# Optimization experiments

Hardware: AMD Instinct MI355X
Metric: run time of the kernel (lower is better)

Reference implementation:

```python
import jax, jax.numpy as jnp
import numpy as np

DIM = 512
NUM_HEADS = 8
HEAD_DIM = DIM // NUM_HEADS
B, S = 2, 2048


def setup_inputs() -> dict:
    key = jax.random.key(0)
    ks = jax.random.split(key, 16)
    scale = 1.0 / np.sqrt(DIM)
    inp = {
        "x": jax.random.normal(ks[0], (B, S, DIM), dtype=jnp.float32),
        "Qexpl": jax.random.normal(ks[1], (B, S, DIM), dtype=jnp.float32),
        "Kexpl": jax.random.normal(ks[2], (B, S, DIM), dtype=jnp.float32),
        "fl": jax.random.uniform(ks[3], (B,), dtype=jnp.float32),
        "fu": jax.random.uniform(ks[4], (B,), dtype=jnp.float32),
        "age": jax.random.uniform(ks[5], (B,), dtype=jnp.float32),
        "gender": jax.random.uniform(ks[6], (B,), dtype=jnp.float32),
        # Linear params: weight stored as [out, in] like torch; y = x @ W.T + b
        "Wq": jax.random.normal(ks[7], (DIM, DIM), dtype=jnp.float32) * scale,
        "bq": jnp.zeros((DIM,), dtype=jnp.float32),
        "Wk": jax.random.normal(ks[8], (DIM, DIM), dtype=jnp.float32) * scale,
        "bk": jnp.zeros((DIM,), dtype=jnp.float32),
        "Wv": jax.random.normal(ks[9], (DIM, DIM), dtype=jnp.float32) * scale,
        "bv": jnp.zeros((DIM,), dtype=jnp.float32),
        "Wo": jax.random.normal(ks[10], (DIM, DIM), dtype=jnp.float32) * scale,
        "bo": jnp.zeros((DIM,), dtype=jnp.float32),
    }
    return inp


def reference(x, Qexpl, Kexpl, fl, fu, age, gender, Wq, bq, Wk, bk, Wv, bv, Wo, bo):
    # drofe_fn is None -> Q/K projections used directly.
    Q = Qexpl @ Wq.T + bq            # [B, S, D]
    K = Kexpl @ Wk.T + bk            # [B, S, D]
    V = x @ Wv.T + bv                # [B, S, D]

    def split_heads(t):  # [B, S, D] -> [B, H, S, hd]
        return t.reshape(B, S, NUM_HEADS, HEAD_DIM).transpose(0, 2, 1, 3)

    Qh, Kh, Vh = split_heads(Q), split_heads(K), split_heads(V)
    scale = 1.0 / np.sqrt(HEAD_DIM).astype(np.float32)
    scores = jnp.einsum("bhqd,bhkd->bhqk", Qh, Kh) * scale  # [B, H, S, S]
    weights = jax.nn.softmax(scores, axis=-1)
    attn = jnp.einsum("bhqk,bhkd->bhqd", weights, Vh)        # [B, H, S, hd]
    attn = attn.transpose(0, 2, 1, 3).reshape(B, S, DIM)
    return attn @ Wo.T + bo
```

## Files before the change

kernel.cpp:

```cpp
#include <hip/hip_runtime.h>
#include <hip/hip_bf16.h>

typedef unsigned short ushort_t;
typedef __attribute__((ext_vector_type(8))) short bf16x8;
typedef __attribute__((ext_vector_type(4))) float f32x4;

__device__ __forceinline__ ushort_t f2bf(float f) {
    union { float f; unsigned u; } v; v.f = f;
    unsigned r = v.u + 0x7FFF + ((v.u >> 16) & 1);
    return (ushort_t)(r >> 16);
}
__device__ __forceinline__ float bfl(ushort_t u) {
    union { unsigned u; float f; } v; v.u = (unsigned)u << 16; return v.f;
}
__device__ __forceinline__ bf16x8 ld8(const ushort_t* p) { return *(const bf16x8*)p; }

__device__ __forceinline__ unsigned cvt2(float x, float y) {
    __hip_bfloat162 h = __float22bfloat162_rn(make_float2(x, y));
    unsigned r; __builtin_memcpy(&r, &h, 4); return r;
}
__device__ __forceinline__ bf16x8 pack8f(float4 a, float4 b) {
    union { unsigned u[4]; bf16x8 v; } o;
    o.u[0] = cvt2(a.x, a.y); o.u[1] = cvt2(a.z, a.w);
    o.u[2] = cvt2(b.x, b.y); o.u[3] = cvt2(b.z, b.w);
    return o.v;
}

__device__ __forceinline__ void gload_lds16(const ushort_t* g, ushort_t* l) {
    __builtin_amdgcn_global_load_lds(
        (const __attribute__((address_space(1))) void*)g,
        (__attribute__((address_space(3))) void*)l, 16, 0, 0);
}

__global__ __launch_bounds__(256, 2)
void proj_qkv_kernel(const float* __restrict__ Qe, const float* __restrict__ Ke,
                     const float* __restrict__ x,
                     const float* __restrict__ Wq, const float* __restrict__ Wk,
                     const float* __restrict__ Wv,
                     const float* __restrict__ bq, const float* __restrict__ bk,
                     const float* __restrict__ bv,
                     ushort_t* __restrict__ Qo, ushort_t* __restrict__ Ko,
                     ushort_t* __restrict__ Vt,
                     const float* __restrict__ Wo, ushort_t* __restrict__ Wob)
{
    const int z = blockIdx.z;
    if (z == 3) {
        int idx = ((blockIdx.y * 4 + blockIdx.x) * 256 + threadIdx.x) * 8;
        const float* s = Wo + idx;
        *(bf16x8*)(Wob + idx) = pack8f(*(const float4*)s, *(const float4*)(s + 4));
        return;
    }

    __shared__ ushort_t smem[2 * 128 * 72];
    ushort_t* lA = smem;
    ushort_t* lB = smem + 128 * 72;

    const float* A = (z == 0) ? Qe : (z == 1) ? Ke : x;
    const float* W = (z == 0) ? Wq : (z == 1) ? Wk : Wv;
    const float* bias = (z == 0) ? bq : (z == 1) ? bk : bv;

    const int m0 = blockIdx.y * 128, n0 = blockIdx.x * 128;
    const int t = threadIdx.x;
    const int lane = t & 63, wave = t >> 6;
    const int wm = (wave & 1) * 64, wn = (wave >> 1) * 64;
    const int fr = lane & 15, quad = lane >> 4;

    f32x4 acc[4][4] = {};
    float4 fa[4][2], fw[4][2];

#pragma unroll
    for (int i = 0; i < 4; ++i) {
        int s = i * 256 + t;
        int r = s >> 3, jp = s & 7;
        const float* pa = A + (size_t)(m0 + r) * 512 + jp * 8;
        fa[i][0] = *(const float4*)pa; fa[i][1] = *(const float4*)(pa + 4);
        const float* pw = W + (size_t)(n0 + r) * 512 + jp * 8;
        fw[i][0] = *(const float4*)pw; fw[i][1] = *(const float4*)(pw + 4);
    }

    for (int kk = 0; kk < 8; ++kk) {
        if (kk) __syncthreads();
#pragma unroll
        for (int i = 0; i < 4; ++i) {
            int s = i * 256 + t;
            int r = s >> 3, jp = s & 7;
            *(bf16x8*)(lA + r * 72 + jp * 8) = pack8f(fa[i][0], fa[i][1]);
            *(bf16x8*)(lB + r * 72 + jp * 8) = pack8f(fw[i][0], fw[i][1]);
        }
        __syncthreads();
        if (kk < 7) {
            int k0 = (kk + 1) * 64;
#pragma unroll
            for (int i = 0; i < 4; ++i) {
                int s = i * 256 + t;
                int r = s >> 3, jp = s & 7;
                const float* pa = A + (size_t)(m0 + r) * 512 + k0 + jp * 8;
                fa[i][0] = *(const float4*)pa; fa[i][1] = *(const float4*)(pa + 4);
                const float* pw = W + (size_t)(n0 + r) * 512 + k0 + jp * 8;
                fw[i][0] = *(const float4*)pw; fw[i][1] = *(const float4*)(pw + 4);
            }
        }

#pragma unroll
        for (int ks = 0; ks < 2; ++ks) {
            bf16x8 af[4], bfrag[4];
#pragma unroll
            for (int mt = 0; mt < 4; ++mt)
                af[mt] = ld8(lA + (wm + mt * 16 + fr) * 72 + (ks * 4 + quad) * 8);
#pragma unroll
            for (int nt = 0; nt < 4; ++nt)
                bfrag[nt] = ld8(lB + (wn + nt * 16 + fr) * 72 + (ks * 4 + quad) * 8);
#pragma unroll
            for (int mt = 0; mt < 4; ++mt)
#pragma unroll
                for (int nt = 0; nt < 4; ++nt)
                    acc[mt][nt] = __builtin_amdgcn_mfma_f32_16x16x32_bf16(
                        af[mt], bfrag[nt], acc[mt][nt], 0, 0, 0);
        }
    }

    const float C1 = 0.125f * 1.44269504088896340736f;
    if (z != 2) {
        ushort_t* dst = (z == 0) ? Qo : Ko;
#pragma unroll
        for (int nt = 0; nt < 4; ++nt) {
            int n = n0 + wn + nt * 16 + fr;
            float bb = bias[n];
#pragma unroll
            for (int mt = 0; mt < 4; ++mt) {
                int mb = m0 + wm + mt * 16 + quad * 4;
                if (z == 0) {
#pragma unroll
                    for (int r = 0; r < 4; ++r)
                        dst[(size_t)(mb + r) * 512 + n] = f2bf((acc[mt][nt][r] + bb) * C1);
                } else {
#pragma unroll
                    for (int r = 0; r < 4; ++r)
                        dst[(size_t)(mb + r) * 512 + n] = f2bf(acc[mt][nt][r] + bb);
                }
            }
        }
    } else {
        __syncthreads();
        ushort_t* lT = smem;
#pragma unroll
        for (int nt = 0; nt < 4; ++nt) {
            int nl = wn + nt * 16 + fr;
            float bb = bias[n0 + nl];
#pragma unroll
            for (int mt = 0; mt < 4; ++mt) {
                int tm = wm + mt * 16 + quad * 4;
#pragma unroll
                for (int r = 0; r < 4; ++r) {
                    int tl = tm + r;
                    int sg = (tl & 96) + ((tl & 12) << 1) + ((tl >> 4 & 1) << 2) + (tl & 3);
                    lT[nl * 136 + sg] = f2bf(acc[mt][nt][r] + bb);
                }
            }
        }
        __syncthreads();
        const int bidx = m0 >> 11, m0t = m0 & 2047;
#pragma unroll
        for (int i = 0; i < 8; ++i) {
            int s = i * 256 + t;
            int row = s >> 4, c = s & 15;
            int n = n0 + row;
            int h = n >> 6, d = n & 63;
            bf16x8 v = ld8(lT + row * 136 + c * 8);
            *(bf16x8*)(Vt + ((size_t)((bidx * 8 + h) * 64 + d)) * 2048 + m0t + c * 8) = v;
        }
    }
}

__global__ __launch_bounds__(256, 2)
void gemm_o_kernel(const ushort_t* __restrict__ Oh, const float* __restrict__ Lsum,
                   const ushort_t* __restrict__ W, const float* __restrict__ bias,
                   float* __restrict__ dst)
{
    __shared__ ushort_t lA[64 * 72];
    __shared__ ushort_t lB[64 * 72];
    const int m0 = blockIdx.y * 64, n0 = blockIdx.x * 64;
    const int t = threadIdx.x;
    const int lane = t & 63, wave = t >> 6;
    const int wm = (wave & 1) * 32, wn = (wave >> 1) * 32;
    const int fr = lane & 15, quad = lane >> 4;
    const int bq_ = m0 >> 11, qq0 = m0 & 2047;

    f32x4 acc[2][2] = {};
    bf16x8 va0[2], va1[2], vw[2];
    float l0[2], l1[2];

#pragma unroll
    for (int i = 0; i < 2; ++i) {
        int s = i * 256 + t;
        int r = s >> 3, jp = s & 7;
        va0[i] = ld8(Oh + (size_t)(m0 + r) * 512 + jp * 8);
        va1[i] = ld8(Oh + (size_t)(m0 + r + 4096) * 512 + jp * 8);
        l0[i] = Lsum[(bq_ * 8 + 0) * 2048 + qq0 + r];
        l1[i] = Lsum[((2 + bq_) * 8 + 0) * 2048 + qq0 + r];
        vw[i] = ld8(W + (size_t)(n0 + r) * 512 + jp * 8);
    }

    for (int kk = 0; kk < 8; ++kk) {
        if (kk) __syncthreads();
#pragma unroll
        for (int i = 0; i < 2; ++i) {
            int s = i * 256 + t;
            int r = s >> 3, jp = s & 7;
            float inv = 1.f / (l0[i] + l1[i]);
            union { bf16x8 v; ushort_t s8[8]; } a0, a1;
            a0.v = va0[i]; a1.v = va1[i];
            union { unsigned u[4]; bf16x8 v; } o;
#pragma unroll
            for (int j = 0; j < 4; ++j)
                o.u[j] = cvt2((bfl(a0.s8[2 * j]) + bfl(a1.s8[2 * j])) * inv,
                              (bfl(a0.s8[2 * j + 1]) + bfl(a1.s8[2 * j + 1])) * inv);
            *(bf16x8*)(lA + r * 72 + jp * 8) = o.v;
            *(bf16x8*)(lB + r * 72 + jp * 8) = vw[i];
        }
        __syncthreads();
        if (kk < 7) {
            int k0 = (kk + 1) * 64;
#pragma unroll
            for (int i = 0; i < 2; ++i) {
                int s = i * 256 + t;
                int r = s >> 3, jp = s & 7;
                va0[i] = ld8(Oh + (size_t)(m0 + r) * 512 + k0 + jp * 8);
                va1[i] = ld8(Oh + (size_t)(m0 + r + 4096) * 512 + k0 + jp * 8);
                l0[i] = Lsum[(bq_ * 8 + kk + 1) * 2048 + qq0 + r];
                l1[i] = Lsum[((2 + bq_) * 8 + kk + 1) * 2048 + qq0 + r];
                vw[i] = ld8(W + (size_t)(n0 + r) * 512 + k0 + jp * 8);
            }
        }

        bf16x8 af[2][2], bfrag[2][2];
#pragma unroll
        for (int ks = 0; ks < 2; ++ks) {
#pragma unroll
            for (int mt = 0; mt < 2; ++mt)
                af[mt][ks] = ld8(lA + (wm + mt * 16 + fr) * 72 + (ks * 4 + quad) * 8);
#pragma unroll
            for (int nt = 0; nt < 2; ++nt)
                bfrag[nt][ks] = ld8(lB + (wn + nt * 16 + fr) * 72 + (ks * 4 + quad) * 8);
        }
#pragma unroll
        for (int ks = 0; ks < 2; ++ks)
#pragma unroll
            for (int mt = 0; mt < 2; ++mt)
#pragma unroll
                for (int nt = 0; nt < 2; ++nt)
                    acc[mt][nt] = __builtin_amdgcn_mfma_f32_16x16x32_bf16(
                        af[mt][ks], bfrag[nt][ks], acc[mt][nt], 0, 0, 0);
    }

#pragma unroll
    for (int nt = 0; nt < 2; ++nt) {
        int n = n0 + wn + nt * 16 + fr;
        float bb = bias[n];
#pragma unroll
        for (int mt = 0; mt < 2; ++mt) {
            int mb = m0 + wm + mt * 16 + quad * 4;
#pragma unroll
            for (int r = 0; r < 4; ++r)
                dst[(size_t)(mb + r) * 512 + n] = acc[mt][nt][r] + bb;
        }
    }
}

__global__ __launch_bounds__(256, 4)
void attn_kernel(const ushort_t* __restrict__ Q, const ushort_t* __restrict__ K,
                 const ushort_t* __restrict__ Vt, ushort_t* __restrict__ Opart,
                 float* __restrict__ Lsum)
{
    __shared__ ushort_t lK[128 * 64];
    __shared__ ushort_t lV[64 * 128];

    const int b = blockIdx.z >> 1, half = blockIdx.z & 1;
    const int h = blockIdx.y;
    const int q0 = blockIdx.x * 64;
    const int kvbase = half * 1024;
    const int t = threadIdx.x;
    const int lane = t & 63, w = t >> 6;
    const int wq = w * 16;
    const int fr = lane & 15, quad = lane >> 4;
    const int fr7 = fr & 7;

    bf16x8 aq[2];
    {
        const ushort_t* qp = Q + (size_t)(b * 2048 + q0 + wq + fr) * 512 + h * 64 + quad * 8;
        aq[0] = ld8(qp);
        aq[1] = ld8(qp + 32);
    }

    const int krl = w * 32 + (lane >> 3);
    const ushort_t* kg = K + (size_t)(b * 2048 + kvbase + krl) * 512 + h * 64
                           + (lane & 7) * 8;
    ushort_t* lk_wr = lK + krl * 64 + (((lane & 7) ^ (krl & 7)) << 3);

    const int vrl = w * 4 + (lane >> 4);
    const ushort_t* vbase = Vt + (size_t)((b * 8 + h) * 64 + vrl) * 2048 + kvbase
                              + (((lane & 15) ^ (vrl & 7)) << 3);

    const ushort_t* kr0 = lK + fr * 64 + ((quad ^ fr7) << 3);
    const ushort_t* kr1 = lK + fr * 64 + (((4 + quad) ^ fr7) << 3);
    const ushort_t* vr0 = lV + fr * 128 + (((0 * 4 + quad) ^ fr7) << 3);
    const ushort_t* vr1 = lV + fr * 128 + (((1 * 4 + quad) ^ fr7) << 3);
    const ushort_t* vr2 = lV + fr * 128 + (((2 * 4 + quad) ^ fr7) << 3);
    const ushort_t* vr3 = lV + fr * 128 + (((3 * 4 + quad) ^ fr7) << 3);
    const ushort_t* vr[4] = { vr0, vr1, vr2, vr3 };

    bf16x8 kreg[4];
#pragma unroll
    for (int i = 0; i < 4; ++i)
        kreg[i] = ld8(kg + (size_t)(i * 8) * 512);
#pragma unroll
    for (int i = 0; i < 4; ++i)
        *(bf16x8*)(lk_wr + i * 8 * 64) = kreg[i];
    __syncthreads();

    f32x4 oacc[4] = {};
    float lsum = 0.f;

    for (int tt = 0; tt < 8; ++tt) {
        const int kv = tt << 7;

#pragma unroll
        for (int i = 0; i < 4; ++i)
            gload_lds16(vbase + kv + (size_t)(i * 16) * 2048, lV + (i * 16 + w * 4) * 128);
        __builtin_amdgcn_sched_barrier(0);
        if (tt < 7) {
#pragma unroll
            for (int i = 0; i < 4; ++i)
                kreg[i] = ld8(kg + (size_t)(kv + 128 + i * 8) * 512);
        }
        __builtin_amdgcn_sched_barrier(0);

        f32x4 sc[8] = {};
        __builtin_amdgcn_s_setprio(1);
#pragma unroll
        for (int nt = 0; nt < 8; ++nt) {
            bf16x8 kb = ld8(kr0 + nt * 16 * 64);
            sc[nt] = __builtin_amdgcn_mfma_f32_16x16x32_bf16(kb, aq[0], sc[nt], 0, 0, 0);
        }
#pragma unroll
        for (int nt = 0; nt < 8; ++nt) {
            bf16x8 kb = ld8(kr1 + nt * 16 * 64);
            sc[nt] = __builtin_amdgcn_mfma_f32_16x16x32_bf16(kb, aq[1], sc[nt], 0, 0, 0);
        }
        __builtin_amdgcn_s_setprio(0);

        if (tt < 7) asm volatile("s_waitcnt vmcnt(4)" ::: "memory");
        else        asm volatile("s_waitcnt vmcnt(0)" ::: "memory");
        __builtin_amdgcn_s_barrier();
        __builtin_amdgcn_sched_barrier(0);

        __builtin_amdgcn_s_setprio(1);
#pragma unroll
        for (int ks = 0; ks < 4; ++ks) {
            float p0[4], p1[4];
#pragma unroll
            for (int r = 0; r < 4; ++r) p0[r] = exp2f(sc[2 * ks][r]);
#pragma unroll
            for (int r = 0; r < 4; ++r) p1[r] = exp2f(sc[2 * ks + 1][r]);
            lsum += ((p0[0] + p0[1]) + (p0[2] + p0[3]))
                  + ((p1[0] + p1[1]) + (p1[2] + p1[3]));
            union { unsigned u[4]; bf16x8 v; } pa;
            pa.u[0] = cvt2(p0[0], p0[1]); pa.u[1] = cvt2(p0[2], p0[3]);
            pa.u[2] = cvt2(p1[0], p1[1]); pa.u[3] = cvt2(p1[2], p1[3]);
#pragma unroll
            for (int nt = 0; nt < 4; ++nt) {
                bf16x8 vb = ld8(vr[ks] + nt * 16 * 128);
                oacc[nt] = __builtin_amdgcn_mfma_f32_16x16x32_bf16(pa.v, vb, oacc[nt], 0, 0, 0);
            }
            if (ks == 0 && tt < 7) {
#pragma unroll
                for (int i = 0; i < 4; ++i)
                    *(bf16x8*)(lk_wr + i * 8 * 64) = kreg[i];
            }
        }
        __builtin_amdgcn_s_setprio(0);
        __syncthreads();
    }

    float rs = lsum;
    rs += __shfl_xor(rs, 16, 64);
    rs += __shfl_xor(rs, 32, 64);
#pragma unroll
    for (int r = 0; r < 4; ++r) {
        int qrow = q0 + wq + quad * 4 + r;
        ushort_t* od = Opart + ((size_t)(half * 2 + b) * 2048 + qrow) * 512 + h * 64;
#pragma unroll
        for (int nt = 0; nt < 4; ++nt)
            od[nt * 16 + fr] = f2bf(oacc[nt][r]);
    }
    if (lane < 16)
        Lsum[((half * 2 + b) * 8 + h) * 2048 + q0 + wq + lane] = rs;
}

extern "C" void kernel_launch(void* const* d_in, const int* in_sizes, int n_in,
                              void* d_out, int out_size, void* d_ws, size_t ws_size,
                              hipStream_t stream) {
    const float* x   = (const float*)d_in[0];
    const float* Qe  = (const float*)d_in[1];
    const float* Ke  = (const float*)d_in[2];
    const float* Wq  = (const float*)d_in[7];
    const float* bq  = (const float*)d_in[8];
    const float* Wk  = (const float*)d_in[9];
    const float* bk  = (const float*)d_in[10];
    const float* Wv  = (const float*)d_in[11];
    const float* bv  = (const float*)d_in[12];
    const float* Wo  = (const float*)d_in[13];
    const float* bo  = (const float*)d_in[14];

    const size_t NTOK = 2 * 2048;
    const size_t ACT = NTOK * 512;

    ushort_t* p = (ushort_t*)d_ws;
    ushort_t* Qws = p; p += ACT;
    ushort_t* Kws = p; p += ACT;
    ushort_t* Vt  = p; p += ACT;
    ushort_t* OpH = p; p += 2 * ACT;
    ushort_t* Wob = p; p += 512 * 512;
    float* Lsum  = (float*)p;

    proj_qkv_kernel<<<dim3(4, 32, 4), 256, 0, stream>>>(Qe, Ke, x, Wq, Wk, Wv,
                                                        bq, bk, bv, Qws, Kws, Vt,
                                                        Wo, Wob);
    attn_kernel<<<dim3(32, 8, 4), 256, 0, stream>>>(Qws, Kws, Vt, OpH, Lsum);
    gemm_o_kernel<<<dim3(8, 64), 256, 0, stream>>>(OpH, Lsum, Wob, bo, (float*)d_out);
}
```

Before: 159.4 us.

## Pre-cast inputs to bf16 and stream projection tiles via direct LDS loads

Adds a separate cast kernel that converts activations and all four weight matrices to bf16 in workspace. The QKV projection then loads bf16 tiles straight into LDS with global_load_lds, double-buffered and XOR-swizzled, instead of loading fp32 into registers and packing per tile. This removes the register staging and conversion from the GEMM loop and overlaps loads with MFMA. The cost is an extra kernel launch plus a full fp32 read and bf16 write/read round trip through memory.

```diff
diff --git a/kernel.cpp b/kernel.cpp
--- a/kernel.cpp
+++ b/kernel.cpp
@@ -32,31 +32,40 @@
         (__attribute__((address_space(3))) void*)l, 16, 0, 0);
 }
 
+__global__ __launch_bounds__(256)
+void cast_kernel(const float* __restrict__ Qe, const float* __restrict__ Ke,
+                 const float* __restrict__ x,  const float* __restrict__ Wq,
+                 const float* __restrict__ Wk, const float* __restrict__ Wv,
+                 const float* __restrict__ Wo,
+                 ushort_t* __restrict__ Ab, ushort_t* __restrict__ Wb)
+{
+    const unsigned i8 = (blockIdx.x * 256u + threadIdx.x) * 8u;
+    const float* src; ushort_t* dst;
+    if (i8 < (3u << 21)) {
+        unsigned a = i8 >> 21, off = i8 & ((1u << 21) - 1);
+        src = (a == 0 ? Qe : a == 1 ? Ke : x) + off;
+        dst = Ab + i8;
+    } else {
+        unsigned j = i8 - (3u << 21);
+        unsigned a = j >> 18, off = j & ((1u << 18) - 1);
+        src = (a == 0 ? Wq : a == 1 ? Wk : a == 2 ? Wv : Wo) + off;
+        dst = Wb + j;
+    }
+    *(bf16x8*)dst = pack8f(*(const float4*)src, *(const float4*)(src + 4));
+}
+
 __global__ __launch_bounds__(256, 2)
-void proj_qkv_kernel(const float* __restrict__ Qe, const float* __restrict__ Ke,
-                     const float* __restrict__ x,
-                     const float* __restrict__ Wq, const float* __restrict__ Wk,
-                     const float* __restrict__ Wv,
+void proj_qkv_kernel(const ushort_t* __restrict__ Ab, const ushort_t* __restrict__ Wb,
                      const float* __restrict__ bq, const float* __restrict__ bk,
                      const float* __restrict__ bv,
                      ushort_t* __restrict__ Qo, ushort_t* __restrict__ Ko,
-                     ushort_t* __restrict__ Vt,
-                     const float* __restrict__ Wo, ushort_t* __restrict__ Wob)
+                     ushort_t* __restrict__ Vt)
 {
+    __shared__ ushort_t smem[4 * 128 * 64];
+
     const int z = blockIdx.z;
-    if (z == 3) {
-        int idx = ((blockIdx.y * 4 + blockIdx.x) * 256 + threadIdx.x) * 8;
-        const float* s = Wo + idx;
-        *(bf16x8*)(Wob + idx) = pack8f(*(const float4*)s, *(const float4*)(s + 4));
-        return;
-    }
-
-    __shared__ ushort_t smem[2 * 128 * 72];
-    ushort_t* lA = smem;
-    ushort_t* lB = smem + 128 * 72;
-
-    const float* A = (z == 0) ? Qe : (z == 1) ? Ke : x;
-    const float* W = (z == 0) ? Wq : (z == 1) ? Wk : Wv;
+    const ushort_t* A = Ab + ((size_t)z << 21);
+    const ushort_t* W = Wb + ((size_t)z << 18);
     const float* bias = (z == 0) ? bq : (z == 1) ? bk : bv;
 
     const int m0 = blockIdx.y * 128, n0 = blockIdx.x * 128;
@@ -64,59 +73,56 @@
     const int lane = t & 63, wave = t >> 6;
     const int wm = (wave & 1) * 64, wn = (wave >> 1) * 64;
     const int fr = lane & 15, quad = lane >> 4;
+    const int fr7 = fr & 7;
+
+    const int srl = wave * 32 + (lane >> 3);
+    const int sch = ((lane & 7) ^ (srl & 7)) << 3;
+    const ushort_t* ag = A + (size_t)(m0 + srl) * 512 + sch;
+    const ushort_t* wg = W + (size_t)(n0 + srl) * 512 + sch;
+    const int dbase = wave * 32 * 64;
 
     f32x4 acc[4][4] = {};
-    float4 fa[4][2], fw[4][2];
-
-#pragma unroll
-    for (int i = 0; i < 4; ++i) {
-        int s = i * 256 + t;
-        int r = s >> 3, jp = s & 7;
-        const float* pa = A + (size_t)(m0 + r) * 512 + jp * 8;
-        fa[i][0] = *(const float4*)pa; fa[i][1] = *(const float4*)(pa + 4);
-        const float* pw = W + (size_t)(n0 + r) * 512 + jp * 8;
-        fw[i][0] = *(const float4*)pw; fw[i][1] = *(const float4*)(pw + 4);
-    }
+
+#pragma unroll
+    for (int i = 0; i < 4; ++i)
+        gload_lds16(ag + (size_t)(i * 8) * 512, smem + dbase + i * 512);
+#pragma unroll
+    for (int i = 0; i < 4; ++i)
+        gload_lds16(wg + (size_t)(i * 8) * 512, smem + 8192 + dbase + i * 512);
+    __syncthreads();
 
     for (int kk = 0; kk < 8; ++kk) {
-        if (kk) __syncthreads();
-#pragma unroll
-        for (int i = 0; i < 4; ++i) {
-            int s = i * 256 + t;
-            int r = s >> 3, jp = s & 7;
-            *(bf16x8*)(lA + r * 72 + jp * 8) = pack8f(fa[i][0], fa[i][1]);
-            *(bf16x8*)(lB + r * 72 + jp * 8) = pack8f(fw[i][0], fw[i][1]);
-        }
-        __syncthreads();
+        ushort_t* cur = smem + ((kk & 1) << 14);
+        ushort_t* nxt = smem + (((kk & 1) ^ 1) << 14);
         if (kk < 7) {
-            int k0 = (kk + 1) * 64;
-#pragma unroll
-            for (int i = 0; i < 4; ++i) {
-                int s = i * 256 + t;
-                int r = s >> 3, jp = s & 7;
-                const float* pa = A + (size_t)(m0 + r) * 512 + k0 + jp * 8;
-                fa[i][0] = *(const float4*)pa; fa[i][1] = *(const float4*)(pa + 4);
-                const float* pw = W + (size_t)(n0 + r) * 512 + k0 + jp * 8;
-                fw[i][0] = *(const float4*)pw; fw[i][1] = *(const float4*)(pw + 4);
-            }
+            int ko = (kk + 1) * 64;
+#pragma unroll
+            for (int i = 0; i < 4; ++i)
+                gload_lds16(ag + ko + (size_t)(i * 8) * 512, nxt + dbase + i * 512);
+#pragma unroll
+            for (int i = 0; i < 4; ++i)
+                gload_lds16(wg + ko + (size_t)(i * 8) * 512, nxt + 8192 + dbase + i * 512);
         }
 
 #pragma unroll
         for (int ks = 0; ks < 2; ++ks) {
-            bf16x8 af[4], bfrag[4];
+            bf16x8 af[4], bfr[4];
 #pragma unroll
             for (int mt = 0; mt < 4; ++mt)
-                af[mt] = ld8(lA + (wm + mt * 16 + fr) * 72 + (ks * 4 + quad) * 8);
+                af[mt] = ld8(cur + (wm + mt * 16 + fr) * 64 + (((ks * 4 + quad) ^ fr7) << 3));
 #pragma unroll
             for (int nt = 0; nt < 4; ++nt)
-                bfrag[nt] = ld8(lB + (wn + nt * 16 + fr) * 72 + (ks * 4 + quad) * 8);
+                bfr[nt] = ld8(cur + 8192 + (wn + nt * 16 + fr) * 64 + (((ks * 4 + quad) ^ fr7) << 3));
 #pragma unroll
             for (int mt = 0; mt < 4; ++mt)
 #pragma unroll
                 for (int nt = 0; nt < 4; ++nt)
                     acc[mt][nt] = __builtin_amdgcn_mfma_f32_16x16x32_bf16(
-                        af[mt], bfrag[nt], acc[mt][nt], 0, 0, 0);
-        }
+                        af[mt], bfr[nt], acc[mt][nt], 0, 0, 0);
+        }
+        asm volatile("s_waitcnt vmcnt(0)" ::: "memory");
+        __builtin_amdgcn_s_barrier();
+        __builtin_amdgcn_sched_barrier(0);
     }
 
     const float C1 = 0.125f * 1.44269504088896340736f;
@@ -141,7 +147,6 @@
             }
         }
     } else {
-        __syncthreads();
         ushort_t* lT = smem;
 #pragma unroll
         for (int nt = 0; nt < 4; ++nt) {
@@ -416,16 +421,18 @@
     const size_t ACT = NTOK * 512;
 
     ushort_t* p = (ushort_t*)d_ws;
+    ushort_t* Abf = p; p += (size_t)3 << 21;
+    ushort_t* Wbf = p; p += (size_t)4 << 18;
     ushort_t* Qws = p; p += ACT;
     ushort_t* Kws = p; p += ACT;
     ushort_t* Vt  = p; p += ACT;
     ushort_t* OpH = p; p += 2 * ACT;
-    ushort_t* Wob = p; p += 512 * 512;
     float* Lsum  = (float*)p;
 
-    proj_qkv_kernel<<<dim3(4, 32, 4), 256, 0, stream>>>(Qe, Ke, x, Wq, Wk, Wv,
-                                                        bq, bk, bv, Qws, Kws, Vt,
-                                                        Wo, Wob);
+    cast_kernel<<<dim3(3584), 256, 0, stream>>>(Qe, Ke, x, Wq, Wk, Wv, Wo, Abf, Wbf);
+    proj_qkv_kernel<<<dim3(4, 32, 3), 256, 0, stream>>>(Abf, Wbf, bq, bk, bv,
+                                                        Qws, Kws, Vt);
     attn_kernel<<<dim3(32, 8, 4), 256, 0, stream>>>(Qws, Kws, Vt, OpH, Lsum);
-    gemm_o_kernel<<<dim3(8, 64), 256, 0, stream>>>(OpH, Lsum, Wob, bo, (float*)d_out);
-}
+    gemm_o_kernel<<<dim3(8, 64), 256, 0, stream>>>(OpH, Lsum, Wbf + ((size_t)3 << 18),
+                                                   bo, (float*)d_out);
+}
```

After: 157.1 us. No clear change (-1.5%).
